# Performance work log

Measured on AMD Instinct MI355X. Metric: run time of the kernel, lower is better.

The kernel has to match this reference:

```python
import jax, jax.numpy as jnp
import numpy as np

EMBED = 1024
NHEAD = 16
HEAD_DIM = EMBED // NHEAD
DFF = 4096
TOP_K = 64
LN_EPS = 1e-5


def _layernorm(x, g, b):
    mu = jnp.mean(x, axis=-1, keepdims=True)
    var = jnp.var(x, axis=-1, keepdims=True)
    return (x - mu) * jax.lax.rsqrt(var + LN_EPS) * g + b


def setup_inputs() -> dict:
    key = jax.random.key(0)
    ks = jax.random.split(key, 12)
    s = 0.02
    return {
        "x": jax.random.normal(ks[0], (2, 2048, EMBED), dtype=jnp.float32),
        "Wq": jax.random.normal(ks[1], (EMBED, EMBED), dtype=jnp.float32) * s,
        "bq": jnp.zeros((EMBED,), jnp.float32),
        "Wk": jax.random.normal(ks[2], (EMBED, EMBED), dtype=jnp.float32) * s,
        "bk": jnp.zeros((EMBED,), jnp.float32),
        "Wv": jax.random.normal(ks[3], (EMBED, EMBED), dtype=jnp.float32) * s,
        "bv": jnp.zeros((EMBED,), jnp.float32),
        "Wo": jax.random.normal(ks[4], (EMBED, EMBED), dtype=jnp.float32) * s,
        "bo": jnp.zeros((EMBED,), jnp.float32),
        "g1": jnp.ones((EMBED,), jnp.float32),
        "be1": jnp.zeros((EMBED,), jnp.float32),
        "g2": jnp.ones((EMBED,), jnp.float32),
        "be2": jnp.zeros((EMBED,), jnp.float32),
        "W1": jax.random.normal(ks[5], (EMBED, DFF), dtype=jnp.float32) * s,
        "b1": jnp.zeros((DFF,), jnp.float32),
        "W2": jax.random.normal(ks[6], (DFF, EMBED), dtype=jnp.float32) * s,
        "b2": jnp.zeros((EMBED,), jnp.float32),
    }


def reference(x, Wq, bq, Wk, bk, Wv, bv, Wo, bo, g1, be1, g2, be2, W1, b1, W2, b2):
    B, N, E = x.shape
    res = x
    h = _layernorm(x, g1, be1)
    # [B, H, N, D]
    q = (h @ Wq + bq).reshape(B, N, NHEAD, HEAD_DIM).transpose(0, 2, 1, 3)
    k = (h @ Wk + bk).reshape(B, N, NHEAD, HEAD_DIM).transpose(0, 2, 1, 3)
    v = (h @ Wv + bv).reshape(B, N, NHEAD, HEAD_DIM).transpose(0, 2, 1, 3)
    scores = jnp.einsum("bhqd,bhkd->bhqk", q, k) / jnp.sqrt(jnp.float32(HEAD_DIM))
    if TOP_K < N:
        topv, _ = jax.lax.top_k(scores, TOP_K)  # [B,H,N,TOP_K]
        thresh = topv[..., -1:, ]
        scores = jnp.where(scores < thresh, -jnp.inf, scores)
    attn = jax.nn.softmax(scores, axis=-1)
    out = jnp.einsum("bhqk,bhkd->bhqd", attn, v)
    out = out.transpose(0, 2, 1, 3).reshape(B, N, E)
    out = out @ Wo + bo
    x1 = res + out  # dropout is identity at eval
    h2 = _layernorm(x1, g2, be2)
    ff = jax.nn.gelu(h2 @ W1 + b1, approximate=False) @ W2 + b2
    return x1 + ff
```

## Files before the change

### kernel.cpp

```cpp
#include <hip/hip_runtime.h>

typedef short short8v __attribute__((ext_vector_type(8)));
typedef float floatx4 __attribute__((ext_vector_type(4)));
typedef unsigned short us4 __attribute__((ext_vector_type(4)));
typedef unsigned short us2 __attribute__((ext_vector_type(2)));

#define EMB 1024
#define QKVW 3072
#define SEQ 2048
#define NH 16
#define HD 64
#define TOPK 64
#define QBLK 16
#define CAP 128
#define SROW 2056
#define QSCALE 0.18033688f
#define ATTN_SMEM (QBLK * SROW * 2 + QBLK * CAP * 4 + 64)

#define GLDS16(gp, lp)                                                        \
  __builtin_amdgcn_global_load_lds(                                           \
      (const __attribute__((address_space(1))) void*)(gp),                    \
      (__attribute__((address_space(3))) void*)(lp), 16, 0, 0)

#if __has_builtin(__builtin_amdgcn_exp2f)
#define EXP2F(x) __builtin_amdgcn_exp2f(x)
#else
#define EXP2F(x) exp2f(x)
#endif

static __device__ __forceinline__ unsigned short f2b(float f) {
  union { float f; unsigned u; } in; in.f = f;
  unsigned u = in.u;
  return (unsigned short)((u + 0x7FFFu + ((u >> 16) & 1u)) >> 16);
}
static __device__ __forceinline__ float b2f(unsigned short b) {
  union { unsigned u; float f; } o; o.u = ((unsigned)b) << 16;
  return o.f;
}
static __device__ __forceinline__ unsigned mmap(unsigned s) {
  return (s & 0x8000u) ? (~s & 0xFFFFu) : (s | 0x8000u);
}
static __device__ __forceinline__ unsigned short munmap(unsigned u) {
  return (u & 0x8000u) ? (unsigned short)(u ^ 0x8000u) : (unsigned short)(~u & 0xFFFFu);
}
static __device__ __forceinline__ unsigned mmap2(unsigned s) {
  const unsigned t = ((s >> 15) & 0x00010001u) * 0x7FFFu;
  return s ^ (0x80008000u | t);
}

__global__ __launch_bounds__(256) void ln_kernel(const float* __restrict__ X,
    const float* __restrict__ gam, const float* __restrict__ bet,
    unsigned short* __restrict__ H) {
  const int row = blockIdx.x;
  const int tid = threadIdx.x;
  const float4 v = *(const float4*)&X[(size_t)row * EMB + tid * 4];
  float s1 = v.x + v.y + v.z + v.w;
  float s2 = v.x * v.x + v.y * v.y + v.z * v.z + v.w * v.w;
#pragma unroll
  for (int off = 32; off; off >>= 1) { s1 += __shfl_xor(s1, off); s2 += __shfl_xor(s2, off); }
  __shared__ float red[2][4];
  const int w = tid >> 6, l = tid & 63;
  if (l == 0) { red[0][w] = s1; red[1][w] = s2; }
  __syncthreads();
  s1 = red[0][0] + red[0][1] + red[0][2] + red[0][3];
  s2 = red[1][0] + red[1][1] + red[1][2] + red[1][3];
  const float mu = s1 * (1.f / EMB);
  const float var = s2 * (1.f / EMB) - mu * mu;
  const float rs = rsqrtf(var + 1e-5f);
  const float4 gv = *(const float4*)&gam[tid * 4];
  const float4 bv = *(const float4*)&bet[tid * 4];
  us4 o;
  o.x = f2b((v.x - mu) * rs * gv.x + bv.x);
  o.y = f2b((v.y - mu) * rs * gv.y + bv.y);
  o.z = f2b((v.z - mu) * rs * gv.z + bv.z);
  o.w = f2b((v.w - mu) * rs * gv.w + bv.w);
  *(us4*)&H[(size_t)row * EMB + tid * 4] = o;
}

__global__ __launch_bounds__(256) void wcvt_all_kernel(
    const float* __restrict__ Wq, const float* __restrict__ Wk,
    const float* __restrict__ Wv, const float* __restrict__ Wo,
    const float* __restrict__ W1, const float* __restrict__ W2,
    const float* __restrict__ bq, const float* __restrict__ bk,
    const float* __restrict__ bv,
    unsigned short* __restrict__ WqkvT, unsigned short* __restrict__ WoT,
    unsigned short* __restrict__ W1T, unsigned short* __restrict__ W2T,
    float* __restrict__ bqkv) {
  const int bid = blockIdx.x;
  const int tid = threadIdx.x;
  if (bid >= 3072) {
    const int i = (bid - 3072) * 256 + tid;
    float v;
    if (i < 1024) v = bq[i] * QSCALE;
    else if (i < 2048) v = bk[i - 1024];
    else v = bv[i - 2048];
    bqkv[i] = v;
    return;
  }
  const float* W; unsigned short* WT; int K, N, t; float scale = 1.f;
  if (bid < 768) {
    const int seg = bid >> 8; t = bid & 255;
    W = (seg == 0) ? Wq : ((seg == 1) ? Wk : Wv);
    WT = WqkvT + (size_t)seg * 1024 * 1024;
    K = 1024; N = 1024;
    if (seg == 0) scale = QSCALE;
  } else if (bid < 1024) {
    t = bid - 768;  W = Wo; WT = WoT; K = 1024; N = 1024;
  } else if (bid < 2048) {
    t = bid - 1024; W = W1; WT = W1T; K = 1024; N = 4096;
  } else {
    t = bid - 2048; W = W2; WT = W2T; K = 4096; N = 1024;
  }
  const int sh = (N == 4096) ? 6 : 4;
  const int n0 = (t & ((1 << sh) - 1)) * 64, k0 = (t >> sh) * 64;
  __shared__ unsigned short tl[64][72];
#pragma unroll
  for (int i = 0; i < 4; ++i) {
    const int f = i * 256 + tid;
    const int k = f >> 4, n4 = (f & 15) * 4;
    const float4 v = *(const float4*)&W[(size_t)(k0 + k) * N + n0 + n4];
    tl[n4 + 0][k] = f2b(v.x * scale);
    tl[n4 + 1][k] = f2b(v.y * scale);
    tl[n4 + 2][k] = f2b(v.z * scale);
    tl[n4 + 3][k] = f2b(v.w * scale);
  }
  __syncthreads();
#pragma unroll
  for (int i = 0; i < 2; ++i) {
    const int f = i * 256 + tid;
    const int n = f >> 3, c8 = (f & 7) * 8;
    short8v o;
#pragma unroll
    for (int j = 0; j < 8; ++j) o[j] = (short)tl[n][c8 + j];
    *(short8v*)&WT[(size_t)(n0 + n) * K + k0 + c8] = o;
  }
}

static __device__ __forceinline__ void xcd_tile(int& bm, int& bn, int tn) {
  const int gx = gridDim.x;
  const int nwg = gx * gridDim.y;
  const int flat = blockIdx.y * gx + blockIdx.x;
  const int q8 = nwg >> 3;
  const int wg = (flat & 7) * q8 + (flat >> 3);
  bm = (wg / gx) * 128;
  bn = (wg % gx) * tn;
}

template <int EPI>
__global__ __launch_bounds__(256) void gemm_bt4_kernel(
    const unsigned short* __restrict__ A, const unsigned short* __restrict__ BT,
    const float* __restrict__ bias, const float* __restrict__ res,
    void* __restrict__ Cout, int M, int N, int K) {
  __shared__ __align__(16) unsigned short lA[2][128 * 32];
  __shared__ __align__(16) unsigned short lB[2][128 * 32];
  const int tid = threadIdx.x;
  const int l = tid & 63, w = tid >> 6;
  const int wm = (w >> 1) * 64, wn = (w & 1) * 64;
  int bm, bn; xcd_tile(bm, bn, 128);
  const int g = l >> 4, r16 = l & 15;
  const int lr = l >> 2, lc = (l & 3) * 8;
  floatx4 acc[4][4] = {};
  const int nt = K >> 5;
#pragma unroll
  for (int j = 0; j < 2; ++j) {
    GLDS16(&A[(size_t)(bm + w * 32 + j * 16 + lr) * K + lc], &lA[0][(w * 32 + j * 16) * 32]);
    GLDS16(&BT[(size_t)(bn + w * 32 + j * 16 + lr) * K + lc], &lB[0][(w * 32 + j * 16) * 32]);
  }
  __syncthreads();
  int cur = 0;
  for (int t = 0; t < nt; ++t) {
    if (t + 1 < nt) {
      const int kt = (t + 1) << 5;
#pragma unroll
      for (int j = 0; j < 2; ++j) {
        GLDS16(&A[(size_t)(bm + w * 32 + j * 16 + lr) * K + kt + lc],
               &lA[cur ^ 1][(w * 32 + j * 16) * 32]);
        GLDS16(&BT[(size_t)(bn + w * 32 + j * 16 + lr) * K + kt + lc],
               &lB[cur ^ 1][(w * 32 + j * 16) * 32]);
      }
    }
    short8v a[4], b[4];
#pragma unroll
    for (int m = 0; m < 4; ++m)
      a[m] = *(const short8v*)&lA[cur][(wm + m * 16 + r16) * 32 + g * 8];
#pragma unroll
    for (int n = 0; n < 4; ++n)
      b[n] = *(const short8v*)&lB[cur][(wn + n * 16 + r16) * 32 + g * 8];
#pragma unroll
    for (int m = 0; m < 4; ++m)
#pragma unroll
      for (int n = 0; n < 4; ++n)
        acc[m][n] = __builtin_amdgcn_mfma_f32_16x16x32_bf16(a[m], b[n], acc[m][n], 0, 0, 0);
    __syncthreads();
    cur ^= 1;
  }
#pragma unroll
  for (int m = 0; m < 4; ++m) {
#pragma unroll
    for (int n = 0; n < 4; ++n) {
#pragma unroll
      for (int r = 0; r < 4; ++r) {
        const int gm = bm + wm + m * 16 + g * 4 + r;
        const int gn = bn + wn + n * 16 + r16;
        float v = acc[m][n][r] + bias[gn];
        if constexpr (EPI == 0) {
          ((unsigned short*)Cout)[(size_t)gm * N + gn] = f2b(v);
        } else if constexpr (EPI == 1) {
          const float ge = 0.5f * v * (1.f + erff(v * 0.70710678118f));
          ((unsigned short*)Cout)[(size_t)gm * N + gn] = f2b(ge);
        } else {
          ((float*)Cout)[(size_t)gm * N + gn] = v + res[(size_t)gm * N + gn];
        }
      }
    }
  }
}

template <int EPI>
__global__ __launch_bounds__(256) void gemm_n64_kernel(
    const unsigned short* __restrict__ A, const unsigned short* __restrict__ BT,
    const float* __restrict__ bias, const float* __restrict__ res,
    void* __restrict__ Cout, int M, int N, int K) {
  __shared__ __align__(16) unsigned short lA[2][128 * 32];
  __shared__ __align__(16) unsigned short lB[2][64 * 32];
  const int tid = threadIdx.x;
  const int l = tid & 63, w = tid >> 6;
  const int wm = (w & 1) * 64, wn = (w >> 1) * 32;
  int bm, bn; xcd_tile(bm, bn, 64);
  const int g = l >> 4, r16 = l & 15;
  const int lr = l >> 2, lc = (l & 3) * 8;
  floatx4 acc[4][2] = {};
  const int nt = K >> 5;
#pragma unroll
  for (int j = 0; j < 2; ++j)
    GLDS16(&A[(size_t)(bm + w * 32 + j * 16 + lr) * K + lc], &lA[0][(w * 32 + j * 16) * 32]);
  GLDS16(&BT[(size_t)(bn + w * 16 + lr) * K + lc], &lB[0][(w * 16) * 32]);
  __syncthreads();
  int cur = 0;
  for (int t = 0; t < nt; ++t) {
    if (t + 1 < nt) {
      const int kt = (t + 1) << 5;
#pragma unroll
      for (int j = 0; j < 2; ++j)
        GLDS16(&A[(size_t)(bm + w * 32 + j * 16 + lr) * K + kt + lc],
               &lA[cur ^ 1][(w * 32 + j * 16) * 32]);
      GLDS16(&BT[(size_t)(bn + w * 16 + lr) * K + kt + lc], &lB[cur ^ 1][(w * 16) * 32]);
    }
    short8v a[4], b[2];
#pragma unroll
    for (int m = 0; m < 4; ++m)
      a[m] = *(const short8v*)&lA[cur][(wm + m * 16 + r16) * 32 + g * 8];
#pragma unroll
    for (int n = 0; n < 2; ++n)
      b[n] = *(const short8v*)&lB[cur][(wn + n * 16 + r16) * 32 + g * 8];
#pragma unroll
    for (int m = 0; m < 4; ++m)
#pragma unroll
      for (int n = 0; n < 2; ++n)
        acc[m][n] = __builtin_amdgcn_mfma_f32_16x16x32_bf16(a[m], b[n], acc[m][n], 0, 0, 0);
    __syncthreads();
    cur ^= 1;
  }
#pragma unroll
  for (int m = 0; m < 4; ++m) {
#pragma unroll
    for (int n = 0; n < 2; ++n) {
#pragma unroll
      for (int r = 0; r < 4; ++r) {
        const int gm = bm + wm + m * 16 + g * 4 + r;
        const int gn = bn + wn + n * 16 + r16;
        float v = acc[m][n][r] + bias[gn];
        if constexpr (EPI == 0) {
          ((unsigned short*)Cout)[(size_t)gm * N + gn] = f2b(v);
        } else if constexpr (EPI == 1) {
          const float ge = 0.5f * v * (1.f + erff(v * 0.70710678118f));
          ((unsigned short*)Cout)[(size_t)gm * N + gn] = f2b(ge);
        } else {
          ((float*)Cout)[(size_t)gm * N + gn] = v + res[(size_t)gm * N + gn];
        }
      }
    }
  }
}

__global__ __launch_bounds__(1024, 8) void attn_kernel(
    const unsigned short* __restrict__ qkv, unsigned short* __restrict__ O) {
  extern __shared__ unsigned short smem[];
  unsigned short (*scores)[SROW] = (unsigned short(*)[SROW])smem;
  unsigned* hist = (unsigned*)(smem + QBLK * SROW);
  unsigned* cnts = (unsigned*)(smem + QBLK * SROW + 4096);

  const int tid = threadIdx.x;
  const int l = tid & 63, w = tid >> 6;
  const int g = l >> 4, r16 = l & 15;
  const int qb = blockIdx.x;
  const int h = blockIdx.y;
  const int bz = blockIdx.z;
  const size_t rowbase = (size_t)bz * SEQ;
  const int hcol = h * HD;

  ((uint2*)hist)[tid] = uint2{0u, 0u};
  if (tid < 16) cnts[tid] = 0u;

  {
    const size_t qrow = (rowbase + qb * QBLK + r16) * QKVW + hcol;
    const short8v qf0 = *(const short8v*)&qkv[qrow + g * 8];
    const short8v qf1 = *(const short8v*)&qkv[qrow + 32 + g * 8];
    const int kbase = w * 128;
#pragma unroll 2
    for (int kti = 0; kti < 8; ++kti) {
      const int key0 = kbase + kti * 16;
      const size_t krow = (rowbase + key0 + r16) * QKVW + 1024 + hcol;
      const short8v kf0 = *(const short8v*)&qkv[krow + g * 8];
      const short8v kf1 = *(const short8v*)&qkv[krow + 32 + g * 8];
      floatx4 acc = {0.f, 0.f, 0.f, 0.f};
      acc = __builtin_amdgcn_mfma_f32_16x16x32_bf16(kf0, qf0, acc, 0, 0, 0);
      acc = __builtin_amdgcn_mfma_f32_16x16x32_bf16(kf1, qf1, acc, 0, 0, 0);
      union { float f; unsigned u; } c0, c1, c2, c3;
      c0.f = acc[0]; c1.f = acc[1]; c2.f = acc[2]; c3.f = acc[3];
      const unsigned p01 = __builtin_amdgcn_perm(c1.u, c0.u, 0x07060302u);
      const unsigned p23 = __builtin_amdgcn_perm(c3.u, c2.u, 0x07060302u);
      uint2 pw; pw.x = mmap2(p01); pw.y = mmap2(p23);
      *(uint2*)&scores[r16][key0 + g * 4] = pw;
    }
  }
  __syncthreads();

  const int quarter = l >> 4, j16 = l & 15;
  const int q = w;
  unsigned* srow32 = (unsigned*)&scores[q][0];
  unsigned* comp = &hist[q * CAP];

  unsigned ux[16];
  us2 mx2 = {0, 0};
#pragma unroll
  for (int i = 0; i < 16; ++i) {
    const unsigned x = srow32[l + 64 * i];
    ux[i] = x;
    union { unsigned u; us2 v; } c; c.u = x;
    mx2 = __builtin_elementwise_max(mx2, c.v);
  }
  unsigned um = (mx2.x > mx2.y) ? (unsigned)mx2.x : (unsigned)mx2.y;
#pragma unroll
  for (int off = 32; off; off >>= 1) {
    const unsigned o2 = (unsigned)__shfl_xor((int)um, off);
    um = (o2 > um) ? o2 : um;
  }
  const float mf = b2f(munmap(um));

#pragma unroll
  for (int i = 0; i < 16; ++i) {
    const unsigned d0 = um - (ux[i] & 0xFFFFu);
    const unsigned d1 = um - (ux[i] >> 16);
    if (d0 < 256u) atomicAdd(&comp[d0 >> 1], 1u << ((d0 & 1u) * 16));
    if (d1 < 256u) atomicAdd(&comp[d1 >> 1], 1u << ((d1 & 1u) * 16));
  }
  asm volatile("s_waitcnt lgkmcnt(0)" ::: "memory");
  unsigned ut;
  {
    const unsigned w0 = comp[2 * l], w1 = comp[2 * l + 1];
    const unsigned c0 = w0 & 0xFFFFu, c1 = w0 >> 16, c2 = w1 & 0xFFFFu, c3 = w1 >> 16;
    const unsigned s4 = c0 + c1 + c2 + c3;
    unsigned incl = s4;
#pragma unroll
    for (int off = 1; off < 64; off <<= 1) {
      const unsigned t2 = (unsigned)__shfl_up((int)incl, off);
      if (l >= off) incl += t2;
    }
    const unsigned pre = incl - s4;
    unsigned dc = 0xFFFFFFFFu;
    if      (pre + c0 >= TOPK)           dc = 4 * l;
    else if (pre + c0 + c1 >= TOPK)      dc = 4 * l + 1;
    else if (pre + c0 + c1 + c2 >= TOPK) dc = 4 * l + 2;
    else if (incl >= TOPK)               dc = 4 * l + 3;
#pragma unroll
    for (int off = 32; off; off >>= 1) {
      const unsigned o2 = (unsigned)__shfl_xor((int)dc, off);
      dc = (o2 < dc) ? o2 : dc;
    }
    if (dc != 0xFFFFFFFFu) {
      ut = um - dc;
    } else {
      unsigned t = 0;
#pragma unroll 1
      for (int bit = 15; bit >= 0; --bit) {
        const unsigned cand = t | (1u << bit);
        int c = 0;
#pragma unroll
        for (int i = 0; i < 16; ++i) {
          c += __popcll(__ballot((ux[i] & 0xFFFFu) >= cand));
          c += __popcll(__ballot((ux[i] >> 16) >= cand));
        }
        if (c >= TOPK) t = cand;
      }
      ut = t;
    }
  }

#pragma unroll
  for (int i = 0; i < 16; ++i) {
    const unsigned u0 = ux[i] & 0xFFFFu, u1 = ux[i] >> 16;
    const unsigned key0 = 2 * (l + 64 * i);
    if (u0 >= ut) {
      const unsigned pos = atomicAdd(&cnts[q], 1u);
      if (pos < CAP) comp[pos] = (key0 << 16) | u0;
    }
    if (u1 >= ut) {
      const unsigned pos = atomicAdd(&cnts[q], 1u);
      if (pos < CAP) comp[pos] = ((key0 + 1) << 16) | u1;
    }
  }
  asm volatile("s_waitcnt lgkmcnt(0)" ::: "memory");
  unsigned cnt = cnts[q];
  asm volatile("s_waitcnt lgkmcnt(0)" ::: "memory");
  cnt = (cnt < CAP) ? cnt : CAP;

  float e0 = 0.f, e1 = 0.f;
  unsigned c0v = 0, c1v = 0;
  const bool h0 = ((unsigned)l < cnt), h1 = ((unsigned)(l + 64) < cnt);
  if (h0) {
    c0v = comp[l];
    e0 = EXP2F(b2f(munmap(c0v & 0xFFFFu)) - mf);
  }
  if (h1) {
    c1v = comp[l + 64];
    e1 = EXP2F(b2f(munmap(c1v & 0xFFFFu)) - mf);
  }
  float lsum = e0 + e1;
#pragma unroll
  for (int off = 32; off; off >>= 1) lsum += __shfl_xor(lsum, off);
  const float rinv = 1.f / lsum;
  if (h0) {
    unsigned pp; asm("v_cvt_pk_bf16_f32 %0, %1, %2" : "=v"(pp) : "v"(e0), "v"(e0));
    comp[l] = (c0v & 0xFFFF0000u) | (pp & 0xFFFFu);
  }
  if (h1) {
    unsigned pp; asm("v_cvt_pk_bf16_f32 %0, %1, %2" : "=v"(pp) : "v"(e1), "v"(e1));
    comp[l + 64] = (c1v & 0xFFFF0000u) | (pp & 0xFFFFu);
  }

  const unsigned short* vbase = &qkv[rowbase * QKVW + 2048 + hcol + j16 * 4];
  float a0 = 0.f, a1 = 0.f, a2 = 0.f, a3 = 0.f;
#pragma unroll 4
  for (int k = 0; k < 16; ++k) {
    const unsigned c = comp[k * 4 + quarter];
    const float p = b2f((unsigned short)(c & 0xFFFFu));
    const unsigned idx = c >> 16;
    const uint2 vv = *(const uint2*)&vbase[(size_t)idx * QKVW];
    union { unsigned u; float f; } t0, t1, t2, t3;
    t0.u = vv.x << 16; t1.u = vv.x & 0xFFFF0000u;
    t2.u = vv.y << 16; t3.u = vv.y & 0xFFFF0000u;
    a0 += p * t0.f; a1 += p * t1.f; a2 += p * t2.f; a3 += p * t3.f;
  }
#pragma unroll 1
  for (unsigned k = 64; k < cnt; k += 4) {
    const unsigned kk = k + quarter;
    const unsigned c = (kk < cnt) ? comp[kk] : 0u;
    const float p = b2f((unsigned short)(c & 0xFFFFu));
    const unsigned idx = c >> 16;
    const uint2 vv = *(const uint2*)&vbase[(size_t)idx * QKVW];
    union { unsigned u; float f; } t0, t1, t2, t3;
    t0.u = vv.x << 16; t1.u = vv.x & 0xFFFF0000u;
    t2.u = vv.y << 16; t3.u = vv.y & 0xFFFF0000u;
    a0 += p * t0.f; a1 += p * t1.f; a2 += p * t2.f; a3 += p * t3.f;
  }
  a0 += __shfl_xor(a0, 16); a0 += __shfl_xor(a0, 32);
  a1 += __shfl_xor(a1, 16); a1 += __shfl_xor(a1, 32);
  a2 += __shfl_xor(a2, 16); a2 += __shfl_xor(a2, 32);
  a3 += __shfl_xor(a3, 16); a3 += __shfl_xor(a3, 32);
  if (l < 16) {
    unsigned w0, w1;
    const float r0 = a0 * rinv, r1 = a1 * rinv, r2 = a2 * rinv, r3 = a3 * rinv;
    asm("v_cvt_pk_bf16_f32 %0, %1, %2" : "=v"(w0) : "v"(r0), "v"(r1));
    asm("v_cvt_pk_bf16_f32 %0, %1, %2" : "=v"(w1) : "v"(r2), "v"(r3));
    uint2 ow; ow.x = w0; ow.y = w1;
    *(uint2*)&O[(rowbase + qb * QBLK + q) * EMB + hcol + j16 * 4] = ow;
  }
}

extern "C" void kernel_launch(void* const* d_in, const int* in_sizes, int n_in,
                              void* d_out, int out_size, void* d_ws, size_t ws_size,
                              hipStream_t stream) {
  (void)in_sizes; (void)n_in; (void)out_size; (void)ws_size;
  const float* x  = (const float*)d_in[0];
  const float* Wq = (const float*)d_in[1];
  const float* bq = (const float*)d_in[2];
  const float* Wk = (const float*)d_in[3];
  const float* bk = (const float*)d_in[4];
  const float* Wv = (const float*)d_in[5];
  const float* bv = (const float*)d_in[6];
  const float* Wo = (const float*)d_in[7];
  const float* bo = (const float*)d_in[8];
  const float* g1 = (const float*)d_in[9];
  const float* be1 = (const float*)d_in[10];
  const float* g2 = (const float*)d_in[11];
  const float* be2 = (const float*)d_in[12];
  const float* W1 = (const float*)d_in[13];
  const float* b1 = (const float*)d_in[14];
  const float* W2 = (const float*)d_in[15];
  const float* b2 = (const float*)d_in[16];
  float* out = (float*)d_out;

  char* ws = (char*)d_ws;
  float* x1 = (float*)ws;
  unsigned short* hbuf  = (unsigned short*)(ws + ((size_t)16 << 20));
  unsigned short* qkvb  = (unsigned short*)(ws + ((size_t)24 << 20));
  unsigned short* Ob    = (unsigned short*)(ws + ((size_t)48 << 20));
  unsigned short* ff1   = (unsigned short*)(ws + ((size_t)24 << 20));
  float* bqkv           = (float*)(ws + ((size_t)48 << 20));
  unsigned short* WqkvT = (unsigned short*)(ws + ((size_t)56 << 20));
  unsigned short* WoT   = (unsigned short*)(ws + ((size_t)62 << 20));
  unsigned short* W1T   = (unsigned short*)(ws + ((size_t)64 << 20));
  unsigned short* W2T   = (unsigned short*)(ws + ((size_t)72 << 20));

  wcvt_all_kernel<<<dim3(3084), 256, 0, stream>>>(Wq, Wk, Wv, Wo, W1, W2, bq, bk, bv,
                                                  WqkvT, WoT, W1T, W2T, bqkv);

  ln_kernel<<<dim3(4096), 256, 0, stream>>>(x, g1, be1, hbuf);
  gemm_bt4_kernel<0><<<dim3(24, 32), 256, 0, stream>>>(hbuf, WqkvT, bqkv, nullptr, qkvb,
                                                       4096, QKVW, 1024);
  (void)hipFuncSetAttribute((const void*)attn_kernel,
                            hipFuncAttributeMaxDynamicSharedMemorySize, ATTN_SMEM);
  attn_kernel<<<dim3(128, 16, 2), 1024, ATTN_SMEM, stream>>>(qkvb, Ob);
  gemm_n64_kernel<2><<<dim3(16, 32), 256, 0, stream>>>(Ob, WoT, bo, x, x1, 4096, 1024, 1024);
  ln_kernel<<<dim3(4096), 256, 0, stream>>>(x1, g2, be2, hbuf);
  gemm_bt4_kernel<1><<<dim3(32, 32), 256, 0, stream>>>(hbuf, W1T, b1, nullptr, ff1,
                                                       4096, 4096, 1024);
  gemm_n64_kernel<2><<<dim3(16, 32), 256, 0, stream>>>(ff1, W2T, b2, x1, out, 4096, 1024, 4096);
}
```

Baseline: 391.3 us.

## Triple-buffer GEMM LDS loads with vmcnt waits and one-wave-per-row layernorm

Both bf16 GEMM kernels move from double to triple-buffered LDS staging. Each iteration prefetches two K-tiles ahead and replaces the full __syncthreads with a partial s_waitcnt vmcnt plus a raw s_barrier, so global-to-LDS loads overlap more of the MFMA work. Layernorm is restructured so one wavefront handles a whole row, with 16 rows per 1024-thread block, which removes the shared-memory cross-wave reduction and its barrier. The triple buffer raises LDS use per block, which may reduce occupancy, and the hand-written vmcnt counts must match the number of loads issued per tile.

```diff
diff --git a/kernel.cpp b/kernel.cpp
--- a/kernel.cpp
+++ b/kernel.cpp
@@ -48,33 +48,42 @@
   return s ^ (0x80008000u | t);
 }
 
-__global__ __launch_bounds__(256) void ln_kernel(const float* __restrict__ X,
+__global__ __launch_bounds__(1024) void ln_kernel(const float* __restrict__ X,
     const float* __restrict__ gam, const float* __restrict__ bet,
     unsigned short* __restrict__ H) {
-  const int row = blockIdx.x;
   const int tid = threadIdx.x;
-  const float4 v = *(const float4*)&X[(size_t)row * EMB + tid * 4];
-  float s1 = v.x + v.y + v.z + v.w;
-  float s2 = v.x * v.x + v.y * v.y + v.z * v.z + v.w * v.w;
+  const int w = tid >> 6, l = tid & 63;
+  const int row = blockIdx.x * 16 + w;
+  const float* xr = &X[(size_t)row * EMB];
+  float4 v0 = *(const float4*)&xr[l * 4];
+  float4 v1 = *(const float4*)&xr[256 + l * 4];
+  float4 v2 = *(const float4*)&xr[512 + l * 4];
+  float4 v3 = *(const float4*)&xr[768 + l * 4];
+  float s1 = (v0.x + v0.y + v0.z + v0.w) + (v1.x + v1.y + v1.z + v1.w) +
+             (v2.x + v2.y + v2.z + v2.w) + (v3.x + v3.y + v3.z + v3.w);
+  float s2 = (v0.x * v0.x + v0.y * v0.y + v0.z * v0.z + v0.w * v0.w) +
+             (v1.x * v1.x + v1.y * v1.y + v1.z * v1.z + v1.w * v1.w) +
+             (v2.x * v2.x + v2.y * v2.y + v2.z * v2.z + v2.w * v2.w) +
+             (v3.x * v3.x + v3.y * v3.y + v3.z * v3.z + v3.w * v3.w);
 #pragma unroll
   for (int off = 32; off; off >>= 1) { s1 += __shfl_xor(s1, off); s2 += __shfl_xor(s2, off); }
-  __shared__ float red[2][4];
-  const int w = tid >> 6, l = tid & 63;
-  if (l == 0) { red[0][w] = s1; red[1][w] = s2; }
-  __syncthreads();
-  s1 = red[0][0] + red[0][1] + red[0][2] + red[0][3];
-  s2 = red[1][0] + red[1][1] + red[1][2] + red[1][3];
   const float mu = s1 * (1.f / EMB);
   const float var = s2 * (1.f / EMB) - mu * mu;
   const float rs = rsqrtf(var + 1e-5f);
-  const float4 gv = *(const float4*)&gam[tid * 4];
-  const float4 bv = *(const float4*)&bet[tid * 4];
-  us4 o;
-  o.x = f2b((v.x - mu) * rs * gv.x + bv.x);
-  o.y = f2b((v.y - mu) * rs * gv.y + bv.y);
-  o.z = f2b((v.z - mu) * rs * gv.z + bv.z);
-  o.w = f2b((v.w - mu) * rs * gv.w + bv.w);
-  *(us4*)&H[(size_t)row * EMB + tid * 4] = o;
+  unsigned short* hr = &H[(size_t)row * EMB];
+#pragma unroll
+  for (int i = 0; i < 4; ++i) {
+    const int c = i * 256 + l * 4;
+    const float4 v = (i == 0) ? v0 : ((i == 1) ? v1 : ((i == 2) ? v2 : v3));
+    const float4 gv = *(const float4*)&gam[c];
+    const float4 bv = *(const float4*)&bet[c];
+    us4 o;
+    o.x = f2b((v.x - mu) * rs * gv.x + bv.x);
+    o.y = f2b((v.y - mu) * rs * gv.y + bv.y);
+    o.z = f2b((v.z - mu) * rs * gv.z + bv.z);
+    o.w = f2b((v.w - mu) * rs * gv.w + bv.w);
+    *(us4*)&hr[c] = o;
+  }
 }
 
 __global__ __launch_bounds__(256) void wcvt_all_kernel(
@@ -151,8 +160,8 @@
     const unsigned short* __restrict__ A, const unsigned short* __restrict__ BT,
     const float* __restrict__ bias, const float* __restrict__ res,
     void* __restrict__ Cout, int M, int N, int K) {
-  __shared__ __align__(16) unsigned short lA[2][128 * 32];
-  __shared__ __align__(16) unsigned short lB[2][128 * 32];
+  __shared__ __align__(16) unsigned short lA[3][128 * 32];
+  __shared__ __align__(16) unsigned short lB[3][128 * 32];
   const int tid = threadIdx.x;
   const int l = tid & 63, w = tid >> 6;
   const int wm = (w >> 1) * 64, wn = (w & 1) * 64;
@@ -166,33 +175,46 @@
     GLDS16(&A[(size_t)(bm + w * 32 + j * 16 + lr) * K + lc], &lA[0][(w * 32 + j * 16) * 32]);
     GLDS16(&BT[(size_t)(bn + w * 32 + j * 16 + lr) * K + lc], &lB[0][(w * 32 + j * 16) * 32]);
   }
-  __syncthreads();
-  int cur = 0;
+#pragma unroll
+  for (int j = 0; j < 2; ++j) {
+    GLDS16(&A[(size_t)(bm + w * 32 + j * 16 + lr) * K + 32 + lc], &lA[1][(w * 32 + j * 16) * 32]);
+    GLDS16(&BT[(size_t)(bn + w * 32 + j * 16 + lr) * K + 32 + lc], &lB[1][(w * 32 + j * 16) * 32]);
+  }
+  asm volatile("s_waitcnt vmcnt(4)" ::: "memory");
+  __builtin_amdgcn_s_barrier();
+  __builtin_amdgcn_sched_barrier(0);
+  int b0 = 0, b1 = 1, b2 = 2;
   for (int t = 0; t < nt; ++t) {
-    if (t + 1 < nt) {
-      const int kt = (t + 1) << 5;
+    const bool pf = (t + 2 < nt);
+    if (pf) {
+      const int kt = (t + 2) << 5;
 #pragma unroll
       for (int j = 0; j < 2; ++j) {
         GLDS16(&A[(size_t)(bm + w * 32 + j * 16 + lr) * K + kt + lc],
-               &lA[cur ^ 1][(w * 32 + j * 16) * 32]);
+               &lA[b2][(w * 32 + j * 16) * 32]);
         GLDS16(&BT[(size_t)(bn + w * 32 + j * 16 + lr) * K + kt + lc],
-               &lB[cur ^ 1][(w * 32 + j * 16) * 32]);
+               &lB[b2][(w * 32 + j * 16) * 32]);
       }
     }
     short8v a[4], b[4];
 #pragma unroll
     for (int m = 0; m < 4; ++m)
-      a[m] = *(const short8v*)&lA[cur][(wm + m * 16 + r16) * 32 + g * 8];
+      a[m] = *(const short8v*)&lA[b0][(wm + m * 16 + r16) * 32 + g * 8];
 #pragma unroll
     for (int n = 0; n < 4; ++n)
-      b[n] = *(const short8v*)&lB[cur][(wn + n * 16 + r16) * 32 + g * 8];
+      b[n] = *(const short8v*)&lB[b0][(wn + n * 16 + r16) * 32 + g * 8];
 #pragma unroll
     for (int m = 0; m < 4; ++m)
 #pragma unroll
       for (int n = 0; n < 4; ++n)
         acc[m][n] = __builtin_amdgcn_mfma_f32_16x16x32_bf16(a[m], b[n], acc[m][n], 0, 0, 0);
-    __syncthreads();
-    cur ^= 1;
+    if (t + 1 < nt) {
+      if (pf) asm volatile("s_waitcnt vmcnt(4)" ::: "memory");
+      else    asm volatile("s_waitcnt vmcnt(0)" ::: "memory");
+      __builtin_amdgcn_s_barrier();
+      __builtin_amdgcn_sched_barrier(0);
+    }
+    const int tmp = b0; b0 = b1; b1 = b2; b2 = tmp;
   }
 #pragma unroll
   for (int m = 0; m < 4; ++m) {
@@ -221,8 +243,8 @@
     const unsigned short* __restrict__ A, const unsigned short* __restrict__ BT,
     const float* __restrict__ bias, const float* __restrict__ res,
     void* __restrict__ Cout, int M, int N, int K) {
-  __shared__ __align__(16) unsigned short lA[2][128 * 32];
-  __shared__ __align__(16) unsigned short lB[2][64 * 32];
+  __shared__ __align__(16) unsigned short lA[3][128 * 32];
+  __shared__ __align__(16) unsigned short lB[3][64 * 32];
   const int tid = threadIdx.x;
   const int l = tid & 63, w = tid >> 6;
   const int wm = (w & 1) * 64, wn = (w >> 1) * 32;
@@ -235,31 +257,43 @@
   for (int j = 0; j < 2; ++j)
     GLDS16(&A[(size_t)(bm + w * 32 + j * 16 + lr) * K + lc], &lA[0][(w * 32 + j * 16) * 32]);
   GLDS16(&BT[(size_t)(bn + w * 16 + lr) * K + lc], &lB[0][(w * 16) * 32]);
-  __syncthreads();
-  int cur = 0;
+#pragma unroll
+  for (int j = 0; j < 2; ++j)
+    GLDS16(&A[(size_t)(bm + w * 32 + j * 16 + lr) * K + 32 + lc], &lA[1][(w * 32 + j * 16) * 32]);
+  GLDS16(&BT[(size_t)(bn + w * 16 + lr) * K + 32 + lc], &lB[1][(w * 16) * 32]);
+  asm volatile("s_waitcnt vmcnt(3)" ::: "memory");
+  __builtin_amdgcn_s_barrier();
+  __builtin_amdgcn_sched_barrier(0);
+  int b0 = 0, b1 = 1, b2 = 2;
   for (int t = 0; t < nt; ++t) {
-    if (t + 1 < nt) {
-      const int kt = (t + 1) << 5;
+    const bool pf = (t + 2 < nt);
+    if (pf) {
+      const int kt = (t + 2) << 5;
 #pragma unroll
       for (int j = 0; j < 2; ++j)
         GLDS16(&A[(size_t)(bm + w * 32 + j * 16 + lr) * K + kt + lc],
-               &lA[cur ^ 1][(w * 32 + j * 16) * 32]);
-      GLDS16(&BT[(size_t)(bn + w * 16 + lr) * K + kt + lc], &lB[cur ^ 1][(w * 16) * 32]);
+               &lA[b2][(w * 32 + j * 16) * 32]);
+      GLDS16(&BT[(size_t)(bn + w * 16 + lr) * K + kt + lc], &lB[b2][(w * 16) * 32]);
     }
     short8v a[4], b[2];
 #pragma unroll
     for (int m = 0; m < 4; ++m)
-      a[m] = *(const short8v*)&lA[cur][(wm + m * 16 + r16) * 32 + g * 8];
+      a[m] = *(const short8v*)&lA[b0][(wm + m * 16 + r16) * 32 + g * 8];
 #pragma unroll
     for (int n = 0; n < 2; ++n)
-      b[n] = *(const short8v*)&lB[cur][(wn + n * 16 + r16) * 32 + g * 8];
+      b[n] = *(const short8v*)&lB[b0][(wn + n * 16 + r16) * 32 + g * 8];
 #pragma unroll
     for (int m = 0; m < 4; ++m)
 #pragma unroll
       for (int n = 0; n < 2; ++n)
         acc[m][n] = __builtin_amdgcn_mfma_f32_16x16x32_bf16(a[m], b[n], acc[m][n], 0, 0, 0);
-    __syncthreads();
-    cur ^= 1;
+    if (t + 1 < nt) {
+      if (pf) asm volatile("s_waitcnt vmcnt(3)" ::: "memory");
+      else    asm volatile("s_waitcnt vmcnt(0)" ::: "memory");
+      __builtin_amdgcn_s_barrier();
+      __builtin_amdgcn_sched_barrier(0);
+    }
+    const int tmp = b0; b0 = b1; b1 = b2; b2 = tmp;
   }
 #pragma unroll
   for (int m = 0; m < 4; ++m) {
@@ -516,14 +550,14 @@
   wcvt_all_kernel<<<dim3(3084), 256, 0, stream>>>(Wq, Wk, Wv, Wo, W1, W2, bq, bk, bv,
                                                   WqkvT, WoT, W1T, W2T, bqkv);
 
-  ln_kernel<<<dim3(4096), 256, 0, stream>>>(x, g1, be1, hbuf);
+  ln_kernel<<<dim3(256), 1024, 0, stream>>>(x, g1, be1, hbuf);
   gemm_bt4_kernel<0><<<dim3(24, 32), 256, 0, stream>>>(hbuf, WqkvT, bqkv, nullptr, qkvb,
                                                        4096, QKVW, 1024);
   (void)hipFuncSetAttribute((const void*)attn_kernel,
                             hipFuncAttributeMaxDynamicSharedMemorySize, ATTN_SMEM);
   attn_kernel<<<dim3(128, 16, 2), 1024, ATTN_SMEM, stream>>>(qkvb, Ob);
   gemm_n64_kernel<2><<<dim3(16, 32), 256, 0, stream>>>(Ob, WoT, bo, x, x1, 4096, 1024, 1024);
-  ln_kernel<<<dim3(4096), 256, 0, stream>>>(x1, g2, be2, hbuf);
+  ln_kernel<<<dim3(256), 1024, 0, stream>>>(x1, g2, be2, hbuf);
   gemm_bt4_kernel<1><<<dim3(32, 32), 256, 0, stream>>>(hbuf, W1T, b1, nullptr, ff1,
                                                        4096, 4096, 1024);
   gemm_n64_kernel<2><<<dim3(16, 32), 256, 0, stream>>>(ff1, W2T, b2, x1, out, 4096, 1024, 4096);
```

New measurement: 398.4 us. No clear change (+1.8%).
